# Performance work log

Measured on AMD Instinct MI355X. Metric: run time of the kernel, lower is better.

## Reference

```python
import jax, jax.numpy as jnp
import numpy as np

B, T, C, H = 2, 2048, 1024, 16
HD = C // H
MAX_WAVELENGTH = 10000.0


def apply_rope(x, positions):
    # x: [B, H, T, HD], positions: [T]
    fraction = 2.0 * jnp.arange(HD // 2, dtype=jnp.float32) / HD
    timescale = MAX_WAVELENGTH ** fraction  # [HD//2]
    sinusoid = positions[:, None] / timescale[None, :]  # [T, HD//2]
    sin = jnp.sin(sinusoid)
    cos = jnp.cos(sinusoid)
    first, second = jnp.split(x, 2, axis=-1)
    out = jnp.concatenate(
        [first * cos - second * sin, second * cos + first * sin], axis=-1
    )
    return out.astype(x.dtype)


def setup_inputs() -> dict:
    key = jax.random.key(0)
    k1, k2, k3 = jax.random.split(key, 3)
    x = jax.random.normal(k1, (B, T, C), dtype=jnp.float32)
    w_attn = jax.random.normal(k2, (C, 3 * C), dtype=jnp.float32) * 0.02
    b_attn = jnp.zeros((3 * C,), dtype=jnp.float32)
    w_proj = jax.random.normal(k3, (C, C), dtype=jnp.float32) * 0.02
    b_proj = jnp.zeros((C,), dtype=jnp.float32)
    return {"x": x, "w_attn": w_attn, "b_attn": b_attn,
            "w_proj": w_proj, "b_proj": b_proj}


def reference(x, w_attn, b_attn, w_proj, b_proj):
    b, t, c = x.shape
    qkv = x @ w_attn + b_attn  # [B, T, 3C]
    q, k, v = jnp.split(qkv, 3, axis=-1)
    q = q.reshape(b, t, H, HD).transpose(0, 2, 1, 3)  # [B, H, T, HD]
    k = k.reshape(b, t, H, HD).transpose(0, 2, 1, 3)
    v = v.reshape(b, t, H, HD).transpose(0, 2, 1, 3)
    positions = jnp.arange(t, dtype=x.dtype)
    q = apply_rope(q, positions)
    k = apply_rope(k, positions)
    att = jnp.einsum('bhqd,bhkd->bhqk', q, k) * (1.0 / jnp.sqrt(HD))
    causal = jnp.tril(jnp.ones((t, t), dtype=bool))
    att = jnp.where(causal, att, jnp.finfo(att.dtype).min)
    att = jax.nn.softmax(att, axis=-1)
    y = jnp.einsum('bhqk,bhkd->bhqd', att, v)
    y = y.transpose(0, 2, 1, 3).reshape(b, t, c)
    return y @ w_proj + b_proj
```

## Files before the change

kernel.cpp:

```cpp
#include <hip/hip_runtime.h>
#include <hip/hip_bf16.h>


typedef __attribute__((ext_vector_type(8))) short short8;
typedef __attribute__((ext_vector_type(4))) float floatx4;

__device__ __forceinline__ unsigned short f2bf(float f) {
    union { float f; unsigned int u; } v; v.f = f;
    unsigned int r = v.u + 0x7FFFu + ((v.u >> 16) & 1u);
    return (unsigned short)(r >> 16);
}

__device__ __forceinline__ unsigned int pk2bf(float a, float b) {
    union { float f; unsigned int u; } ua, ub;
    ua.f = a; ub.f = b;
    return __builtin_amdgcn_perm(ub.u + 0x8000u, ua.u + 0x8000u, 0x07060302u);
}

__device__ __forceinline__ void gld16(const void* g, void* l) {
    __builtin_amdgcn_global_load_lds(
        (const __attribute__((address_space(1))) unsigned int*)g,
        (__attribute__((address_space(3))) unsigned int*)l, 16, 0, 0);
}

__device__ __forceinline__ void transpose_body(
    const float* __restrict__ in, unsigned short* __restrict__ out,
    int R, int NC, int bx, int by, int tid,
    unsigned short (*tile)[65]) {
    int r0 = by * 64, c0 = bx * 64;
    int col = tid & 63, rr = tid >> 6;
#pragma unroll
    for (int i = 0; i < 16; i++) {
        int row = rr + i * 4;
        tile[row][col] = f2bf(in[(size_t)(r0 + row) * NC + c0 + col]);
    }
    __syncthreads();
#pragma unroll
    for (int i = 0; i < 16; i++) {
        int orow = rr + i * 4;
        out[(size_t)(c0 + orow) * R + r0 + col] = tile[col][orow];
    }
}

__global__ __launch_bounds__(256) void prep(
    const float* __restrict__ x,
    const float* __restrict__ w_attn,
    const float* __restrict__ w_proj,
    unsigned short* __restrict__ x_bf,
    unsigned short* __restrict__ wTa,
    unsigned short* __restrict__ wTp,
    float2* __restrict__ tab) {
    __shared__ unsigned short tile[64][65];
    int bid = blockIdx.x;
    int tid = threadIdx.x;
    if (bid < 4096) {
        int i = bid * 256 + tid;
        float4 v = ((const float4*)x)[i];
        ushort4 o;
        o.x = f2bf(v.x); o.y = f2bf(v.y); o.z = f2bf(v.z); o.w = f2bf(v.w);
        ((ushort4*)x_bf)[i] = o;
    } else if (bid < 4864) {
        int t = bid - 4096;
        transpose_body(w_attn, wTa, 1024, 3072, t % 48, t / 48, tid, tile);
    } else if (bid < 5120) {
        int t = bid - 4864;
        transpose_body(w_proj, wTp, 1024, 1024, t & 15, t >> 4, tid, tile);
    } else {
        int i = (bid - 5120) * 256 + tid;
        int t = i >> 5, d = i & 31;
        float inv_ts = exp2f(-0.41524101186092036f * (float)d);
        float ang = (float)t * inv_ts;
        tab[i] = make_float2(sinf(ang), cosf(ang));
    }
}

__global__ __launch_bounds__(256) void gemm_qkv(
    const unsigned short* __restrict__ A,
    const unsigned short* __restrict__ BT,
    const float* __restrict__ bias,
    const float2* __restrict__ tab,
    unsigned short* __restrict__ qT,
    unsigned short* __restrict__ kT,
    unsigned short* __restrict__ vT) {
    __shared__ __align__(16) unsigned short smem[32768];
    int tid = threadIdx.x;
    int lane = tid & 63;
    int w = tid >> 6;
    int wx = w & 1, wy = w >> 1;
    int l16 = lane & 15, quad = lane >> 4;
    int m0 = blockIdx.y * 128;
    int n0 = blockIdx.x * 128;
    int x = l16 & 7;
    int lr = lane >> 3;
    int gc = (lane & 7) ^ lr;

    floatx4 acc[4][4];
#pragma unroll
    for (int mi = 0; mi < 4; mi++)
#pragma unroll
        for (int ni = 0; ni < 4; ni++)
            acc[mi][ni] = (floatx4){0.f, 0.f, 0.f, 0.f};

    auto stage = [&](int bsel, int k0) {
        unsigned short* as = smem + bsel * 16384;
        unsigned short* bs = as + 8192;
#pragma unroll
        for (int i = 0; i < 4; i++) {
            int seg = w * 4 + i;
            int row = seg * 8 + lr;
            gld16(A + (size_t)(m0 + row) * 1024 + k0 + gc * 8, &as[seg * 512]);
            gld16(BT + (size_t)(n0 + row) * 1024 + k0 + gc * 8, &bs[seg * 512]);
        }
    };

    auto compute = [&](int bsel) {
        const unsigned short* as = smem + bsel * 16384;
        const unsigned short* bs = as + 8192;
#pragma unroll
        for (int kk = 0; kk < 2; kk++) {
            short8 af[4], bf[4];
#pragma unroll
            for (int mi = 0; mi < 4; mi++) {
                int r = wy * 64 + mi * 16 + l16;
                af[mi] = *(const short8*)&as[r * 64 + (((kk << 2) | quad) ^ x) * 8];
            }
#pragma unroll
            for (int ni = 0; ni < 4; ni++) {
                int r = wx * 64 + ni * 16 + l16;
                bf[ni] = *(const short8*)&bs[r * 64 + (((kk << 2) | quad) ^ x) * 8];
            }
#pragma unroll
            for (int mi = 0; mi < 4; mi++)
#pragma unroll
                for (int ni = 0; ni < 4; ni++)
                    acc[mi][ni] = __builtin_amdgcn_mfma_f32_16x16x32_bf16(
                        af[mi], bf[ni], acc[mi][ni], 0, 0, 0);
        }
    };

    stage(0, 0);
    __syncthreads();
    int cur = 0;
    for (int k0 = 0; k0 < 960; k0 += 64) {
        stage(cur ^ 1, k0 + 64);
        compute(cur);
        __syncthreads();
        cur ^= 1;
    }
    compute(cur);
    __syncthreads();

    int region = n0 >> 10;
    int b = m0 >> 11;
    float b0 = bias[n0 + wx * 64 + l16];
    float b1 = bias[n0 + wx * 64 + 16 + l16];
    float b2 = bias[n0 + wx * 64 + 32 + l16];
    float b3 = bias[n0 + wx * 64 + 48 + l16];

    if (region < 2) {
        unsigned short* qk = region ? kT : qT;
        float scale = region ? 1.0f : 0.125f;
        unsigned short* lq = smem;
#pragma unroll
        for (int mi = 0; mi < 4; mi++)
#pragma unroll
            for (int r = 0; r < 4; r++) {
                int tl = wy * 64 + mi * 16 + quad * 4 + r;
                int t = (m0 & 2047) + tl;
                float2 sc0 = tab[t * 32 + l16];
                float2 sc1 = tab[t * 32 + 16 + l16];
                float v1 = acc[mi][0][r] + b0, v2 = acc[mi][2][r] + b2;
                float w1 = acc[mi][1][r] + b1, w2 = acc[mi][3][r] + b3;
                unsigned short* orow = lq + tl * 136 + wx * 64;
                orow[l16]      = f2bf((v1 * sc0.y - v2 * sc0.x) * scale);
                orow[l16 + 32] = f2bf((v2 * sc0.y + v1 * sc0.x) * scale);
                orow[l16 + 16] = f2bf((w1 * sc1.y - w2 * sc1.x) * scale);
                orow[l16 + 48] = f2bf((w2 * sc1.y + w1 * sc1.x) * scale);
            }
        __syncthreads();
        int c8 = tid & 7;
        int hl = (tid >> 3) & 1;
        int tl0 = tid >> 4;
        int h = ((n0 & 1023) >> 6) + hl;
        unsigned short* ob = qk + (size_t)(b * 16 + h) * 2048 * 64;
#pragma unroll
        for (int p = 0; p < 8; p++) {
            int tl = p * 16 + tl0;
            int t = (m0 & 2047) + tl;
            short8 val = *(const short8*)&lq[tl * 136 + hl * 64 + c8 * 8];
            *(short8*)&ob[(size_t)t * 64 + c8 * 8] = val;
        }
    } else {
#pragma unroll
        for (int mi = 0; mi < 4; mi++)
#pragma unroll
            for (int ni = 0; ni < 4; ni++) {
                int d_loc = wx * 64 + ni * 16 + l16;
                int t_base = wy * 64 + mi * 16 + quad * 4;
                float bv = (ni == 0) ? b0 : (ni == 1) ? b1 : (ni == 2) ? b2 : b3;
                uint2 pk;
                pk.x = pk2bf(acc[mi][ni][0] + bv, acc[mi][ni][1] + bv);
                pk.y = pk2bf(acc[mi][ni][2] + bv, acc[mi][ni][3] + bv);
                int e = d_loc * 128 + (t_base ^ ((d_loc & 15) << 3));
                *(uint2*)&smem[e] = pk;
            }
        __syncthreads();
        int d_r = tid >> 1, half = tid & 1;
        int cv = (n0 - 2048) + d_r;
        int hh = cv >> 6, dd = cv & 63;
        int fofs = (d_r & 15) << 3;
        size_t vbase = ((size_t)(b * 16 + hh) * 64 + dd) * 2048 + (m0 & 2047);
#pragma unroll
        for (int c = 0; c < 8; c++) {
            int tc = half * 64 + c * 8;
            short8 val = *(const short8*)&smem[d_r * 128 + (tc ^ fofs)];
            *(short8*)&vT[vbase + tc] = val;
        }
    }
}

__global__ __launch_bounds__(256) void gemm_proj(
    const unsigned short* __restrict__ A,
    const unsigned short* __restrict__ BT,
    const float* __restrict__ bias,
    float* __restrict__ out) {
    __shared__ __align__(16) unsigned short smem[24576];
    int lane = threadIdx.x & 63;
    int w = threadIdx.x >> 6;
    int wx = w & 1, wy = w >> 1;
    int l16 = lane & 15, quad = lane >> 4;
    int m0 = blockIdx.y * 128;
    int n0 = blockIdx.x * 64;
    int x = l16 & 7;
    int lr = lane >> 3;
    int gc = (lane & 7) ^ lr;

    floatx4 acc[4][2];
#pragma unroll
    for (int mi = 0; mi < 4; mi++)
#pragma unroll
        for (int ni = 0; ni < 2; ni++)
            acc[mi][ni] = (floatx4){0.f, 0.f, 0.f, 0.f};

    auto stage = [&](int bsel, int k0) {
        unsigned short* as = smem + bsel * 12288;
        unsigned short* bs = as + 8192;
#pragma unroll
        for (int i = 0; i < 6; i++) {
            int seg = w * 6 + i;
            if (seg < 16) {
                int row = seg * 8 + lr;
                gld16(A + (size_t)(m0 + row) * 1024 + k0 + gc * 8, &as[seg * 512]);
            } else {
                int s2 = seg - 16;
                int row = s2 * 8 + lr;
                gld16(BT + (size_t)(n0 + row) * 1024 + k0 + gc * 8, &bs[s2 * 512]);
            }
        }
    };

    auto compute = [&](int bsel) {
        const unsigned short* as = smem + bsel * 12288;
        const unsigned short* bs = as + 8192;
#pragma unroll
        for (int kk = 0; kk < 2; kk++) {
            short8 af[4], bf[2];
#pragma unroll
            for (int mi = 0; mi < 4; mi++) {
                int r = wy * 64 + mi * 16 + l16;
                af[mi] = *(const short8*)&as[r * 64 + (((kk << 2) | quad) ^ x) * 8];
            }
#pragma unroll
            for (int ni = 0; ni < 2; ni++) {
                int r = wx * 32 + ni * 16 + l16;
                bf[ni] = *(const short8*)&bs[r * 64 + (((kk << 2) | quad) ^ x) * 8];
            }
#pragma unroll
            for (int mi = 0; mi < 4; mi++)
#pragma unroll
                for (int ni = 0; ni < 2; ni++)
                    acc[mi][ni] = __builtin_amdgcn_mfma_f32_16x16x32_bf16(
                        af[mi], bf[ni], acc[mi][ni], 0, 0, 0);
        }
    };

    stage(0, 0);
    __syncthreads();
    int cur = 0;
    for (int k0 = 0; k0 < 960; k0 += 64) {
        stage(cur ^ 1, k0 + 64);
        compute(cur);
        __syncthreads();
        cur ^= 1;
    }
    compute(cur);

#pragma unroll
    for (int mi = 0; mi < 4; mi++)
#pragma unroll
        for (int ni = 0; ni < 2; ni++) {
            int row = m0 + wy * 64 + mi * 16 + quad * 4;
            int col = n0 + wx * 32 + ni * 16 + l16;
            float bv = bias[col];
#pragma unroll
            for (int r = 0; r < 4; r++)
                out[(size_t)(row + r) * 1024 + col] = acc[mi][ni][r] + bv;
        }
}

__global__ __launch_bounds__(512) void attn4(
    const unsigned short* __restrict__ qT,
    const unsigned short* __restrict__ kT,
    const unsigned short* __restrict__ vT,
    unsigned short* __restrict__ y) {
    __shared__ __align__(16) unsigned short kbuf[2][64 * 64];
    __shared__ __align__(16) unsigned short vbuf[2][64 * 64];
    __shared__ __align__(16) unsigned short pl[8][16 * 88];
    int lane = threadIdx.x & 63;
    int w = threadIdx.x >> 6;
    int l16 = lane & 15, quad = lane >> 4;
    int blk = blockIdx.x;
    int idx = blk >> 5;
    int qb = (idx < 8) ? (15 - idx * 2) : ((idx - 8) * 2);
    int bh = blk & 31;
    int b = bh >> 4, h = bh & 15;
    int q0 = qb * 128 + w * 16;
    int dt = 2 * qb + (w >> 2);
    const unsigned short* qp = qT + (size_t)bh * 2048 * 64;
    const unsigned short* kp = kT + (size_t)bh * 2048 * 64;
    const unsigned short* vp = vT + (size_t)bh * 64 * 2048;
    unsigned short* plw = pl[w];
    int x = l16 & 7;

    short8 qf0 = *(const short8*)(qp + (size_t)(q0 + l16) * 64 + quad * 8);
    short8 qf1 = *(const short8*)(qp + (size_t)(q0 + l16) * 64 + 32 + quad * 8);

    floatx4 acc[4];
#pragma unroll
    for (int ni = 0; ni < 4; ni++) acc[ni] = (floatx4){0.f, 0.f, 0.f, 0.f};
    float l_part = 0.f;

    auto stage = [&](int bi, int j0) {
#pragma unroll
        for (int i = 0; i < 2; i++) {
            int t = w * 2 + i;
            if (t < 8) {
                int r = t * 8 + (lane >> 3);
                int c = (lane & 7) ^ (r & 7);
                gld16(kp + (size_t)(j0 + r) * 64 + c * 8, &kbuf[bi][t * 512]);
            } else {
                int s = t - 8;
                int d = s * 8 + (lane >> 3);
                int c = (lane & 7) ^ (d & 7);
                gld16(vp + (size_t)d * 2048 + j0 + c * 8, &vbuf[bi][s * 512]);
            }
        }
    };

    int L = 2 * qb + 2;
    stage(0, 0);
    for (int it = 0; it < L; it++) {
        int j0 = it * 64;
        int bi = it & 1;
        __syncthreads();
        if (it + 1 < L) stage(bi ^ 1, j0 + 64);
        if (it > dt) continue;
        const unsigned short* kb = kbuf[bi];
        const unsigned short* vb = vbuf[bi];
        bool diag = (it == dt);
        floatx4 s[4];
#pragma unroll
        for (int c = 0; c < 4; c++) {
            int r = c * 16 + l16;
            short8 kf0 = *(const short8*)&kb[r * 64 + ((quad) ^ x) * 8];
            short8 kf1 = *(const short8*)&kb[r * 64 + ((quad | 4) ^ x) * 8];
            floatx4 z = (floatx4){0.f, 0.f, 0.f, 0.f};
            z = __builtin_amdgcn_mfma_f32_16x16x32_bf16(kf0, qf0, z, 0, 0, 0);
            z = __builtin_amdgcn_mfma_f32_16x16x32_bf16(kf1, qf1, z, 0, 0, 0);
            s[c] = z;
        }
        int query = q0 + l16;
#pragma unroll
        for (int c = 0; c < 4; c++) {
            float p[4];
#pragma unroll
            for (int r = 0; r < 4; r++) {
                float e = __expf(s[c][r]);
                if (diag) {
                    int key = j0 + c * 16 + quad * 4 + r;
                    e = (key <= query) ? e : 0.f;
                }
                p[r] = e;
            }
            l_part += (p[0] + p[1]) + (p[2] + p[3]);
            uint2 pk = {pk2bf(p[0], p[1]), pk2bf(p[2], p[3])};
            *(uint2*)&plw[l16 * 88 + c * 16 + quad * 4] = pk;
        }
        short8 pa0 = *(const short8*)&plw[l16 * 88 + quad * 8];
        short8 pa1 = *(const short8*)&plw[l16 * 88 + 32 + quad * 8];
#pragma unroll
        for (int ni = 0; ni < 4; ni++) {
            int d = ni * 16 + l16;
            short8 vf0 = *(const short8*)&vb[d * 64 + ((quad) ^ x) * 8];
            short8 vf1 = *(const short8*)&vb[d * 64 + ((quad | 4) ^ x) * 8];
            acc[ni] = __builtin_amdgcn_mfma_f32_16x16x32_bf16(pa0, vf0, acc[ni], 0, 0, 0);
            acc[ni] = __builtin_amdgcn_mfma_f32_16x16x32_bf16(pa1, vf1, acc[ni], 0, 0, 0);
        }
    }

    float tot = l_part;
    tot += __shfl_xor(tot, 16, 64);
    tot += __shfl_xor(tot, 32, 64);
    float inv[4];
#pragma unroll
    for (int r = 0; r < 4; r++)
        inv[r] = 1.f / __shfl(tot, quad * 4 + r, 16);
#pragma unroll
    for (int ni = 0; ni < 4; ni++)
#pragma unroll
        for (int r = 0; r < 4; r++) {
            int t = q0 + quad * 4 + r;
            y[((size_t)(b * 2048 + t)) * 1024 + h * 64 + ni * 16 + l16] =
                f2bf(acc[ni][r] * inv[r]);
        }
}

extern "C" void kernel_launch(void* const* d_in, const int* in_sizes, int n_in,
                              void* d_out, int out_size, void* d_ws, size_t ws_size,
                              hipStream_t stream) {
    const float* x      = (const float*)d_in[0];
    const float* w_attn = (const float*)d_in[1];
    const float* b_attn = (const float*)d_in[2];
    const float* w_proj = (const float*)d_in[3];
    const float* b_proj = (const float*)d_in[4];
    float* out = (float*)d_out;

    char* ws = (char*)d_ws;
    unsigned short* x_bf = (unsigned short*)ws;
    unsigned short* wTa  = (unsigned short*)(ws + (8ull << 20));
    unsigned short* wTp  = (unsigned short*)(ws + (14ull << 20));
    unsigned short* qTb  = (unsigned short*)(ws + (16ull << 20));
    unsigned short* kTb  = (unsigned short*)(ws + (24ull << 20));
    unsigned short* vTb  = (unsigned short*)(ws + (32ull << 20));
    float2*         tab  = (float2*)(ws + (40ull << 20));
    unsigned short* y_bf = x_bf;

    prep<<<5376, 256, 0, stream>>>(x, w_attn, w_proj, x_bf, wTa, wTp, tab);
    gemm_qkv<<<dim3(24, 32), 256, 0, stream>>>(x_bf, wTa, b_attn, tab,
                                               qTb, kTb, vTb);
    attn4<<<512, 512, 0, stream>>>(qTb, kTb, vTb, y_bf);
    gemm_proj<<<dim3(16, 32), 256, 0, stream>>>(y_bf, wTp, b_proj, out);
}
```

Baseline: 182.0 us.

## Restructure attention into 64-query blocks with exp2, MFMA row sums, and priorities

The attention kernel now uses 256-thread blocks, each handling 64 queries, with 1024 blocks ordered longest-first. This removes the wasted iterations where half the waves skipped K/V tiles in the old 128-query layout. The log2(e) factor is folded into the Q scale so the kernel can use native exp2. The softmax denominator is computed with an MFMA against a vector of ones instead of per-lane sums and shuffles. It also adds hardware bf16 pack conversion, precomputed staging pointers, and s_setprio around the MFMA sections; the trade-off is that each block reuses K/V over fewer queries, so more loads are issued per query.

```diff
diff --git a/kernel.cpp b/kernel.cpp
--- a/kernel.cpp
+++ b/kernel.cpp
@@ -15,6 +15,12 @@
     union { float f; unsigned int u; } ua, ub;
     ua.f = a; ub.f = b;
     return __builtin_amdgcn_perm(ub.u + 0x8000u, ua.u + 0x8000u, 0x07060302u);
+}
+
+__device__ __forceinline__ unsigned int cvtpk(float a, float b) {
+    unsigned int r;
+    asm("v_cvt_pk_bf16_f32 %0, %1, %2" : "=v"(r) : "v"(a), "v"(b));
+    return r;
 }
 
 __device__ __forceinline__ void gld16(const void* g, void* l) {
@@ -159,7 +165,7 @@
 
     if (region < 2) {
         unsigned short* qk = region ? kT : qT;
-        float scale = region ? 1.0f : 0.125f;
+        float scale = region ? 1.0f : 0.18033688011112042f;
         unsigned short* lq = smem;
 #pragma unroll
         for (int mi = 0; mi < 4; mi++)
@@ -308,67 +314,86 @@
         }
 }
 
-__global__ __launch_bounds__(512) void attn4(
+__global__ __launch_bounds__(256) void attn5(
     const unsigned short* __restrict__ qT,
     const unsigned short* __restrict__ kT,
     const unsigned short* __restrict__ vT,
     unsigned short* __restrict__ y) {
     __shared__ __align__(16) unsigned short kbuf[2][64 * 64];
     __shared__ __align__(16) unsigned short vbuf[2][64 * 64];
-    __shared__ __align__(16) unsigned short pl[8][16 * 88];
+    __shared__ __align__(16) unsigned short pl[4][16 * 72];
     int lane = threadIdx.x & 63;
     int w = threadIdx.x >> 6;
     int l16 = lane & 15, quad = lane >> 4;
     int blk = blockIdx.x;
-    int idx = blk >> 5;
-    int qb = (idx < 8) ? (15 - idx * 2) : ((idx - 8) * 2);
+    int t = 31 - (blk >> 5);
     int bh = blk & 31;
     int b = bh >> 4, h = bh & 15;
-    int q0 = qb * 128 + w * 16;
-    int dt = 2 * qb + (w >> 2);
+    int q0 = t * 64 + w * 16;
     const unsigned short* qp = qT + (size_t)bh * 2048 * 64;
-    const unsigned short* kp = kT + (size_t)bh * 2048 * 64;
-    const unsigned short* vp = vT + (size_t)bh * 64 * 2048;
     unsigned short* plw = pl[w];
     int x = l16 & 7;
 
     short8 qf0 = *(const short8*)(qp + (size_t)(q0 + l16) * 64 + quad * 8);
     short8 qf1 = *(const short8*)(qp + (size_t)(q0 + l16) * 64 + 32 + quad * 8);
 
+    short8 ones;
+#pragma unroll
+    for (int j = 0; j < 8; j++) ones[j] = (short)0x3F80;
+
     floatx4 acc[4];
 #pragma unroll
     for (int ni = 0; ni < 4; ni++) acc[ni] = (floatx4){0.f, 0.f, 0.f, 0.f};
-    float l_part = 0.f;
-
-    auto stage = [&](int bi, int j0) {
-#pragma unroll
-        for (int i = 0; i < 2; i++) {
-            int t = w * 2 + i;
-            if (t < 8) {
-                int r = t * 8 + (lane >> 3);
-                int c = (lane & 7) ^ (r & 7);
-                gld16(kp + (size_t)(j0 + r) * 64 + c * 8, &kbuf[bi][t * 512]);
-            } else {
-                int s = t - 8;
-                int d = s * 8 + (lane >> 3);
-                int c = (lane & 7) ^ (d & 7);
-                gld16(vp + (size_t)d * 2048 + j0 + c * 8, &vbuf[bi][s * 512]);
-            }
+    floatx4 accl = (floatx4){0.f, 0.f, 0.f, 0.f};
+
+    int lr8 = lane >> 3, l8 = lane & 7;
+    const unsigned short* sp[4];
+    unsigned short* ld0[4];
+    int gstep;
+    if (w < 2) {
+        const unsigned short* kp = kT + (size_t)bh * 2048 * 64;
+#pragma unroll
+        for (int i = 0; i < 4; i++) {
+            int seg = w * 4 + i;
+            int row = seg * 8 + lr8;
+            int c = l8 ^ (row & 7);
+            sp[i] = kp + (size_t)row * 64 + c * 8;
+            ld0[i] = &kbuf[0][seg * 512];
+        }
+        gstep = 4096;
+    } else {
+        const unsigned short* vp = vT + (size_t)bh * 64 * 2048;
+#pragma unroll
+        for (int i = 0; i < 4; i++) {
+            int s = (w - 2) * 4 + i;
+            int d = s * 8 + lr8;
+            int c = l8 ^ (d & 7);
+            sp[i] = vp + (size_t)d * 2048 + c * 8;
+            ld0[i] = &vbuf[0][s * 512];
+        }
+        gstep = 64;
+    }
+
+    auto stage = [&](int bi) {
+#pragma unroll
+        for (int i = 0; i < 4; i++) {
+            gld16(sp[i], ld0[i] + bi * 4096);
+            sp[i] += gstep;
         }
     };
 
-    int L = 2 * qb + 2;
-    stage(0, 0);
+    int L = t + 1;
+    int query = q0 + l16;
+    stage(0);
+    int cur = 0;
     for (int it = 0; it < L; it++) {
-        int j0 = it * 64;
-        int bi = it & 1;
         __syncthreads();
-        if (it + 1 < L) stage(bi ^ 1, j0 + 64);
-        if (it > dt) continue;
-        const unsigned short* kb = kbuf[bi];
-        const unsigned short* vb = vbuf[bi];
-        bool diag = (it == dt);
-        floatx4 s[4];
+        if (it + 1 < L) stage(cur ^ 1);
+        const unsigned short* kb = kbuf[cur];
+        const unsigned short* vb = vbuf[cur];
+        bool diag = (it == t);
+        floatx4 s4[4];
+        __builtin_amdgcn_s_setprio(1);
 #pragma unroll
         for (int c = 0; c < 4; c++) {
             int r = c * 16 + l16;
@@ -377,27 +402,32 @@
             floatx4 z = (floatx4){0.f, 0.f, 0.f, 0.f};
             z = __builtin_amdgcn_mfma_f32_16x16x32_bf16(kf0, qf0, z, 0, 0, 0);
             z = __builtin_amdgcn_mfma_f32_16x16x32_bf16(kf1, qf1, z, 0, 0, 0);
-            s[c] = z;
-        }
-        int query = q0 + l16;
+            s4[c] = z;
+        }
+        __builtin_amdgcn_s_setprio(0);
+        int j0 = it * 64;
 #pragma unroll
         for (int c = 0; c < 4; c++) {
             float p[4];
 #pragma unroll
             for (int r = 0; r < 4; r++) {
-                float e = __expf(s[c][r]);
+                float e = __builtin_amdgcn_exp2f(s4[c][r]);
                 if (diag) {
                     int key = j0 + c * 16 + quad * 4 + r;
                     e = (key <= query) ? e : 0.f;
                 }
                 p[r] = e;
             }
-            l_part += (p[0] + p[1]) + (p[2] + p[3]);
-            uint2 pk = {pk2bf(p[0], p[1]), pk2bf(p[2], p[3])};
-            *(uint2*)&plw[l16 * 88 + c * 16 + quad * 4] = pk;
-        }
-        short8 pa0 = *(const short8*)&plw[l16 * 88 + quad * 8];
-        short8 pa1 = *(const short8*)&plw[l16 * 88 + 32 + quad * 8];
+            uint2 pk;
+            pk.x = cvtpk(p[0], p[1]);
+            pk.y = cvtpk(p[2], p[3]);
+            *(uint2*)&plw[l16 * 72 + c * 16 + quad * 4] = pk;
+        }
+        short8 pa0 = *(const short8*)&plw[l16 * 72 + quad * 8];
+        short8 pa1 = *(const short8*)&plw[l16 * 72 + 32 + quad * 8];
+        __builtin_amdgcn_s_setprio(1);
+        accl = __builtin_amdgcn_mfma_f32_16x16x32_bf16(pa0, ones, accl, 0, 0, 0);
+        accl = __builtin_amdgcn_mfma_f32_16x16x32_bf16(pa1, ones, accl, 0, 0, 0);
 #pragma unroll
         for (int ni = 0; ni < 4; ni++) {
             int d = ni * 16 + l16;
@@ -406,21 +436,19 @@
             acc[ni] = __builtin_amdgcn_mfma_f32_16x16x32_bf16(pa0, vf0, acc[ni], 0, 0, 0);
             acc[ni] = __builtin_amdgcn_mfma_f32_16x16x32_bf16(pa1, vf1, acc[ni], 0, 0, 0);
         }
-    }
-
-    float tot = l_part;
-    tot += __shfl_xor(tot, 16, 64);
-    tot += __shfl_xor(tot, 32, 64);
+        __builtin_amdgcn_s_setprio(0);
+        cur ^= 1;
+    }
+
     float inv[4];
 #pragma unroll
-    for (int r = 0; r < 4; r++)
-        inv[r] = 1.f / __shfl(tot, quad * 4 + r, 16);
+    for (int r = 0; r < 4; r++) inv[r] = 1.f / accl[r];
 #pragma unroll
     for (int ni = 0; ni < 4; ni++)
 #pragma unroll
         for (int r = 0; r < 4; r++) {
-            int t = q0 + quad * 4 + r;
-            y[((size_t)(b * 2048 + t)) * 1024 + h * 64 + ni * 16 + l16] =
+            int tr = q0 + quad * 4 + r;
+            y[((size_t)(b * 2048 + tr)) * 1024 + h * 64 + ni * 16 + l16] =
                 f2bf(acc[ni][r] * inv[r]);
         }
 }
@@ -448,6 +476,6 @@
     prep<<<5376, 256, 0, stream>>>(x, w_attn, w_proj, x_bf, wTa, wTp, tab);
     gemm_qkv<<<dim3(24, 32), 256, 0, stream>>>(x_bf, wTa, b_attn, tab,
                                                qTb, kTb, vTb);
-    attn4<<<512, 512, 0, stream>>>(qTb, kTb, vTb, y_bf);
+    attn5<<<1024, 256, 0, stream>>>(qTb, kTb, vTb, y_bf);
     gemm_proj<<<dim3(16, 32), 256, 0, stream>>>(y_bf, wTp, b_proj, out);
 }
```

New measurement: 171.7 us. 1.06x faster.
